# Performance work log

Measured on AMD Instinct MI355X. Metric: run time of the kernel, lower is better.

## Reference

```python
import jax, jax.numpy as jnp
import numpy as np

T, B, I, H, L, O = 512, 64, 128, 512, 2, 256


def _lstm_layer(x, Wih, Whh, b):
    """One LSTM layer over time. x:[T,B,in] -> (ys:[T,B,H], hT:[B,H], cT:[B,H]).
    PyTorch gate order: i, f, g, o. Zero initial state (module's zero buffers)."""
    Hs = Whh.shape[1]
    # Precompute input contribution for all timesteps (one big GEMM).
    xg = jnp.einsum('tbi,gi->tbg', x, Wih) + b  # [T,B,4H]

    def step(carry, xt):
        h, c = carry
        g = xt + h @ Whh.T  # [B,4H]
        i, f, gg, o = jnp.split(g, 4, axis=-1)
        c = jax.nn.sigmoid(f) * c + jax.nn.sigmoid(i) * jnp.tanh(gg)
        h = jax.nn.sigmoid(o) * jnp.tanh(c)
        return (h, c), h

    h0 = jnp.zeros((x.shape[1], Hs), x.dtype)
    (hT, cT), ys = jax.lax.scan(step, (h0, h0), xg)
    return ys, hT, cT


def setup_inputs() -> dict:
    key = jax.random.key(0)
    ks = jax.random.split(key, 9)
    s = 1.0 / np.sqrt(H)  # torch default uniform(-1/sqrt(H), 1/sqrt(H)) scale
    u = lambda k, shp: jax.random.uniform(k, shp, jnp.float32, -s, s)
    return {
        'x': jax.random.normal(ks[0], (T, B, I), jnp.float32),
        'W_ih0': u(ks[1], (4 * H, I)),
        'W_hh0': u(ks[2], (4 * H, H)),
        'b0': u(ks[3], (4 * H,)),  # b_ih + b_hh combined
        'W_ih1': u(ks[4], (4 * H, H)),
        'W_hh1': u(ks[5], (4 * H, H)),
        'b1': u(ks[6], (4 * H,)),
        'fc_w': u(ks[7], (O, H)),
        'fc_b': u(ks[8], (O,)),
    }


def reference(x, W_ih0, W_hh0, b0, W_ih1, W_hh1, b1, fc_w, fc_b):
    y0, h0, c0 = _lstm_layer(x, W_ih0, W_hh0, b0)
    y1, h1, c1 = _lstm_layer(y0, W_ih1, W_hh1, b1)
    fc = jnp.einsum('tbh,oh->tbo', y1, fc_w) + fc_b  # fused output projection
    hN = jnp.stack([h0, h1])  # [L,B,H]
    cN = jnp.stack([c0, c1])
    return fc, (hN, cN)
```

## Files before the change

kernel.cpp:

```cpp
#include <hip/hip_runtime.h>
#include <hip/hip_bf16.h>

#define T_SEQ 512
#define BATCH 64
#define IN0   128
#define HID   512
#define OUTF  256
#define G4    (4*HID)
#define NWG_L 64
#define FLAG_STRIDE 32

typedef __attribute__((ext_vector_type(8))) short short8;
typedef __attribute__((ext_vector_type(4))) float f32x4;
typedef unsigned short u16;

__device__ __forceinline__ float sigmoidf_(float x) { return 1.f / (1.f + __expf(-x)); }
__device__ __forceinline__ float tanhf_(float x)    { return 1.f - 2.f / (1.f + __expf(2.f * x)); }

__device__ __forceinline__ u16 f2bf(float f) {
    union { float f; unsigned u; } a; a.f = f;
    unsigned u = a.u;
    return (u16)((u + 0x7fffu + ((u >> 16) & 1u)) >> 16);
}

__device__ __forceinline__ void wave_poll_ge(unsigned* flags, int lane, unsigned tgt) {
    unsigned it = 0;
    for (;;) {
        unsigned v = __hip_atomic_load(flags + (size_t)lane * FLAG_STRIDE,
                                       __ATOMIC_RELAXED, __HIP_MEMORY_SCOPE_AGENT);
        if (__all((int)(v >= tgt))) return;
        __builtin_amdgcn_s_sleep(2);
        if ((++it & 2047u) == 0u)
            (void)__hip_atomic_load(flags, __ATOMIC_ACQUIRE, __HIP_MEMORY_SCOPE_AGENT);
    }
}

__global__ void cvt_f32_bf16(const float* __restrict__ in, u16* __restrict__ out, int n4) {
    int i = blockIdx.x * blockDim.x + threadIdx.x;
    if (i < n4) {
        float4 v = reinterpret_cast<const float4*>(in)[i];
        ushort4 o;
        o.x = f2bf(v.x); o.y = f2bf(v.y); o.z = f2bf(v.z); o.w = f2bf(v.w);
        reinterpret_cast<ushort4*>(out)[i] = o;
    }
}

template<int LAYER>
__device__ __forceinline__ void run_layer(
    const u16* __restrict__ asrc,
    const u16* __restrict__ wih, const u16* __restrict__ whh,
    const float* __restrict__ bias,
    u16* __restrict__ ybuf,
    float* __restrict__ hNout, float* __restrict__ cNout,
    unsigned* flags_own, unsigned* flags_dep, int g,
    u16 (*lds_w)[32][512], float (*lds_g)[33], float (*lds_b)[16])
{
    constexpr int KIN = (LAYER == 0) ? IN0 : HID;
    constexpr int KS1 = KIN / 32;
    constexpr int KS  = KS1 + 16;

    const int tid  = threadIdx.x;
    const int lane = tid & 63;
    const int w    = tid >> 6;
    const int ubase = 8 * g;

    for (int idx = tid; idx < 2 * KS * 64; idx += 256) {
        int nt  = (idx >= KS * 64) ? 1 : 0;
        int rem = idx - nt * KS * 64;
        int ks = rem >> 6, s = rem & 63, q = s & 15, kq = s >> 4;
        int r = (q >> 2) * HID + ubase + 4 * nt + (q & 3);
        const u16* src = (ks < KS1)
            ? wih + (size_t)r * KIN + (size_t)ks * 32 + kq * 8
            : whh + (size_t)r * HID + (size_t)(ks - KS1) * 32 + kq * 8;
        *reinterpret_cast<uint4*>(&lds_w[nt][ks][s * 8]) =
            *reinterpret_cast<const uint4*>(src);
    }
    if (tid < 32) {
        int nt = tid >> 4, q = tid & 15;
        lds_b[nt][q] = bias[(q >> 2) * HID + ubase + 4 * nt + (q & 3)];
    }
    __syncthreads();

    const int pb  = tid & 63;
    const int pu2 = tid >> 6;
    float c0 = 0.f, c1 = 0.f;

    const int arow = 16 * w + (lane & 15);
    const int koff = (lane >> 4) * 8;

    for (int t = 0; t < T_SEQ; ++t) {
        f32x4 ac0[4] = {{0,0,0,0},{0,0,0,0},{0,0,0,0},{0,0,0,0}};
        f32x4 ac1[4] = {{0,0,0,0},{0,0,0,0},{0,0,0,0},{0,0,0,0}};

        if (LAYER == 0) {
            const u16* ap = asrc + ((size_t)t * BATCH + arow) * KIN + koff;
            short8 a[KS1];
            #pragma unroll
            for (int j = 0; j < KS1; ++j)
                a[j] = *reinterpret_cast<const short8*>(ap + j * 32);
            #pragma unroll
            for (int j = 0; j < KS1; ++j) {
                ac0[j & 3] = __builtin_amdgcn_mfma_f32_16x16x32_bf16(
                    a[j], *reinterpret_cast<const short8*>(&lds_w[0][j][lane * 8]), ac0[j & 3], 0, 0, 0);
                ac1[j & 3] = __builtin_amdgcn_mfma_f32_16x16x32_bf16(
                    a[j], *reinterpret_cast<const short8*>(&lds_w[1][j][lane * 8]), ac1[j & 3], 0, 0, 0);
            }
        }

        if (LAYER == 0) {
            if (t > 0) {
                if (w == 0) wave_poll_ge(flags_own, lane, (unsigned)t);
                __syncthreads();
            }
        } else {
            if (w == 0) wave_poll_ge(flags_own, lane, (unsigned)t);
            if (w == 1) wave_poll_ge(flags_dep, lane, (unsigned)(t + 1));
            __syncthreads();
        }

        if (t > 0) {
            const u16* hp = ybuf + ((size_t)(t - 1) * BATCH + arow) * HID + koff;
            short8 a[16];
            #pragma unroll
            for (int j = 0; j < 16; ++j)
                a[j] = *reinterpret_cast<const short8*>(hp + j * 32);
            #pragma unroll
            for (int j = 0; j < 16; ++j) {
                ac0[j & 3] = __builtin_amdgcn_mfma_f32_16x16x32_bf16(
                    a[j], *reinterpret_cast<const short8*>(&lds_w[0][KS1 + j][lane * 8]), ac0[j & 3], 0, 0, 0);
                ac1[j & 3] = __builtin_amdgcn_mfma_f32_16x16x32_bf16(
                    a[j], *reinterpret_cast<const short8*>(&lds_w[1][KS1 + j][lane * 8]), ac1[j & 3], 0, 0, 0);
            }
        }

        if (LAYER == 1) {
            const u16* ap = asrc + ((size_t)t * BATCH + arow) * HID + koff;
            short8 a[16];
            #pragma unroll
            for (int j = 0; j < 16; ++j)
                a[j] = *reinterpret_cast<const short8*>(ap + j * 32);
            #pragma unroll
            for (int j = 0; j < 16; ++j) {
                ac0[j & 3] = __builtin_amdgcn_mfma_f32_16x16x32_bf16(
                    a[j], *reinterpret_cast<const short8*>(&lds_w[0][j][lane * 8]), ac0[j & 3], 0, 0, 0);
                ac1[j & 3] = __builtin_amdgcn_mfma_f32_16x16x32_bf16(
                    a[j], *reinterpret_cast<const short8*>(&lds_w[1][j][lane * 8]), ac1[j & 3], 0, 0, 0);
            }
        }

        f32x4 s0 = (ac0[0] + ac0[1]) + (ac0[2] + ac0[3]);
        f32x4 s1 = (ac1[0] + ac1[1]) + (ac1[2] + ac1[3]);
        #pragma unroll
        for (int j = 0; j < 4; ++j) {
            int row = 16 * w + (lane >> 4) * 4 + j;
            lds_g[row][lane & 15]        = s0[j];
            lds_g[row][16 + (lane & 15)] = s1[j];
        }
        __syncthreads();

        {
            const int nt = pu2 >> 1;
            const int dq = (2 * pu2) & 3;
            const float* gr = &lds_g[pb][nt * 16];
            const float* br = lds_b[nt];
            float gi0 = sigmoidf_(gr[dq]      + br[dq]);
            float gf0 = sigmoidf_(gr[4 + dq]  + br[4 + dq]);
            float gg0 = tanhf_(   gr[8 + dq]  + br[8 + dq]);
            float go0 = sigmoidf_(gr[12 + dq] + br[12 + dq]);
            c0 = gf0 * c0 + gi0 * gg0;
            float h0v = go0 * tanhf_(c0);
            float gi1 = sigmoidf_(gr[dq + 1]      + br[dq + 1]);
            float gf1 = sigmoidf_(gr[4 + dq + 1]  + br[4 + dq + 1]);
            float gg1 = tanhf_(   gr[8 + dq + 1]  + br[8 + dq + 1]);
            float go1 = sigmoidf_(gr[12 + dq + 1] + br[12 + dq + 1]);
            c1 = gf1 * c1 + gi1 * gg1;
            float h1v = go1 * tanhf_(c1);

            unsigned pack = (unsigned)f2bf(h0v) | ((unsigned)f2bf(h1v) << 16);
            unsigned* yp32 = reinterpret_cast<unsigned*>(ybuf)
                           + ((size_t)t * BATCH + pb) * (HID / 2) + (ubase + 2 * pu2) / 2;
            __hip_atomic_store(yp32, pack, __ATOMIC_RELAXED, __HIP_MEMORY_SCOPE_AGENT);

            if (t == T_SEQ - 1) {
                hNout[pb * HID + ubase + 2 * pu2]     = h0v;
                hNout[pb * HID + ubase + 2 * pu2 + 1] = h1v;
                cNout[pb * HID + ubase + 2 * pu2]     = c0;
                cNout[pb * HID + ubase + 2 * pu2 + 1] = c1;
            }
        }

        asm volatile("s_waitcnt vmcnt(0)" ::: "memory");
        __syncthreads();
        if (tid == 0)
            __hip_atomic_store(flags_own + (size_t)g * FLAG_STRIDE, (unsigned)(t + 1),
                               __ATOMIC_RELAXED, __HIP_MEMORY_SCOPE_AGENT);
    }
}

__global__ __launch_bounds__(256, 1)
void lstm_fused(const u16* __restrict__ x_bf,
                const u16* __restrict__ wih0, const u16* __restrict__ whh0, const float* __restrict__ b0,
                const u16* __restrict__ wih1, const u16* __restrict__ whh1, const float* __restrict__ b1,
                u16* __restrict__ y0, u16* __restrict__ y1,
                float* __restrict__ hN, float* __restrict__ cN,
                unsigned* __restrict__ ctr)
{
    __shared__ __align__(16) u16 lds_w[2][32][512];
    __shared__ float lds_g[BATCH][33];
    __shared__ float lds_b[2][16];

    unsigned* flags0 = ctr;
    unsigned* flags1 = ctr + NWG_L * FLAG_STRIDE;

    const int wgid = blockIdx.x;
    if (wgid < NWG_L) {
        run_layer<0>(x_bf, wih0, whh0, b0, y0, hN, cN,
                     flags0, flags0, wgid, lds_w, lds_g, lds_b);
    } else {
        run_layer<1>(y0, wih1, whh1, b1, y1, hN + BATCH * HID, cN + BATCH * HID,
                     flags1, flags0, wgid - NWG_L, lds_w, lds_g, lds_b);
    }
}

__global__ __launch_bounds__(256)
void fc_kernel(const u16* __restrict__ y1, const u16* __restrict__ fcw,
               const float* __restrict__ fcb, float* __restrict__ out)
{
    const int tid  = threadIdx.x;
    const int lane = tid & 63;
    const int wgid = blockIdx.x * 4 + (tid >> 6);
    const int nq   = wgid & 3;
    const int mt0  = wgid >> 2;

    for (int j = 0; j < 8; ++j) {
        int mt = mt0 + j * 256;
        f32x4 acc[4] = {{0,0,0,0},{0,0,0,0},{0,0,0,0},{0,0,0,0}};
        const u16* arow = y1 + ((size_t)mt * 16 + (lane & 15)) * HID + (lane >> 4) * 8;
        #pragma unroll
        for (int ks = 0; ks < 16; ++ks) {
            short8 a = *reinterpret_cast<const short8*>(arow + ks * 32);
            #pragma unroll
            for (int nt = 0; nt < 4; ++nt) {
                const u16* brow = fcw + ((size_t)(nq * 64 + nt * 16 + (lane & 15))) * HID
                                      + ks * 32 + (lane >> 4) * 8;
                short8 b = *reinterpret_cast<const short8*>(brow);
                acc[nt] = __builtin_amdgcn_mfma_f32_16x16x32_bf16(a, b, acc[nt], 0, 0, 0);
            }
        }
        #pragma unroll
        for (int nt = 0; nt < 4; ++nt) {
            int col = nq * 64 + nt * 16 + (lane & 15);
            float bb = fcb[col];
            #pragma unroll
            for (int jj = 0; jj < 4; ++jj) {
                int row = mt * 16 + (lane >> 4) * 4 + jj;
                out[(size_t)row * OUTF + col] = acc[nt][jj] + bb;
            }
        }
    }
}

extern "C" void kernel_launch(void* const* d_in, const int* in_sizes, int n_in,
                              void* d_out, int out_size, void* d_ws, size_t ws_size,
                              hipStream_t stream)
{
    const float* x    = (const float*)d_in[0];
    const float* wih0 = (const float*)d_in[1];
    const float* whh0 = (const float*)d_in[2];
    const float* b0   = (const float*)d_in[3];
    const float* wih1 = (const float*)d_in[4];
    const float* whh1 = (const float*)d_in[5];
    const float* b1   = (const float*)d_in[6];
    const float* fcw  = (const float*)d_in[7];
    const float* fcb  = (const float*)d_in[8];
    float* out = (float*)d_out;

    const size_t flag_bytes = (size_t)2 * NWG_L * FLAG_STRIDE * 4;

    char* ws = (char*)d_ws;
    size_t off = 0;
    unsigned* ctr = (unsigned*)ws;                    off += flag_bytes;
    u16* x_bf    = (u16*)(ws + off);                  off += (size_t)T_SEQ * BATCH * IN0 * 2;
    u16* wih0_bf = (u16*)(ws + off);                  off += (size_t)G4 * IN0 * 2;
    u16* whh0_bf = (u16*)(ws + off);                  off += (size_t)G4 * HID * 2;
    u16* wih1_bf = (u16*)(ws + off);                  off += (size_t)G4 * HID * 2;
    u16* whh1_bf = (u16*)(ws + off);                  off += (size_t)G4 * HID * 2;
    u16* fcw_bf  = (u16*)(ws + off);                  off += (size_t)OUTF * HID * 2;
    u16* y0      = (u16*)(ws + off);                  off += (size_t)T_SEQ * BATCH * HID * 2;
    u16* y1      = (u16*)(ws + off);                  off += (size_t)T_SEQ * BATCH * HID * 2;

    hipMemsetAsync(ctr, 0, flag_bytes, stream);

    auto conv = [&](const float* in, u16* o, int n) {
        int n4 = n / 4;
        cvt_f32_bf16<<<(n4 + 255) / 256, 256, 0, stream>>>(in, o, n4);
    };
    conv(x,    x_bf,    T_SEQ * BATCH * IN0);
    conv(wih0, wih0_bf, G4 * IN0);
    conv(whh0, whh0_bf, G4 * HID);
    conv(wih1, wih1_bf, G4 * HID);
    conv(whh1, whh1_bf, G4 * HID);
    conv(fcw,  fcw_bf,  OUTF * HID);

    float* outFC = out;
    float* hN = out + (size_t)T_SEQ * BATCH * OUTF;
    float* cN = hN + 2 * BATCH * HID;

    lstm_fused<<<2 * NWG_L, 256, 0, stream>>>(x_bf, wih0_bf, whh0_bf, b0,
                                              wih1_bf, whh1_bf, b1,
                                              y0, y1, hN, cN, ctr);
    fc_kernel<<<256, 256, 0, stream>>>(y1, fcw_bf, fcb, outFC);
}
```

Before: 3.669 ms.

## Pin each LSTM layer's workgroups to one XCD and poll flags via local L2

```diff
diff --git a/kernel.cpp b/kernel.cpp
--- a/kernel.cpp
+++ b/kernel.cpp
@@ -8,7 +8,7 @@
 #define OUTF  256
 #define G4    (4*HID)
 #define NWG_L 64
-#define FLAG_STRIDE 32
+#define FSTR  32
 
 typedef __attribute__((ext_vector_type(8))) short short8;
 typedef __attribute__((ext_vector_type(4))) float f32x4;
@@ -23,15 +23,36 @@
     return (u16)((u + 0x7fffu + ((u >> 16) & 1u)) >> 16);
 }
 
-__device__ __forceinline__ void wave_poll_ge(unsigned* flags, int lane, unsigned tgt) {
-    unsigned it = 0;
+__device__ __forceinline__ unsigned ld_flag_sc0(const unsigned* p) {
+    unsigned v;
+    asm volatile("global_load_dword %0, %1, off sc0\n\ts_waitcnt vmcnt(0)"
+                 : "=v"(v) : "v"(p) : "memory");
+    return v;
+}
+
+__device__ __forceinline__ void poll_local(const unsigned* lf, const unsigned* mf,
+                                           int lane, unsigned tgt) {
+    unsigned best = 0, it = 0;
     for (;;) {
-        unsigned v = __hip_atomic_load(flags + (size_t)lane * FLAG_STRIDE,
+        unsigned v = ld_flag_sc0(lf + (size_t)lane * FSTR);
+        best = v > best ? v : best;
+        if (__all((int)(best >= tgt))) return;
+        if ((++it & 15u) == 0u) {
+            unsigned m = __hip_atomic_load(mf + (size_t)lane * FSTR,
+                                           __ATOMIC_RELAXED, __HIP_MEMORY_SCOPE_AGENT);
+            best = m > best ? m : best;
+            if (__all((int)(best >= tgt))) return;
+        }
+        __builtin_amdgcn_s_sleep(1);
+    }
+}
+
+__device__ __forceinline__ void poll_agent(const unsigned* flags, int lane, unsigned tgt) {
+    for (;;) {
+        unsigned v = __hip_atomic_load(flags + (size_t)lane * FSTR,
                                        __ATOMIC_RELAXED, __HIP_MEMORY_SCOPE_AGENT);
         if (__all((int)(v >= tgt))) return;
         __builtin_amdgcn_s_sleep(2);
-        if ((++it & 2047u) == 0u)
-            (void)__hip_atomic_load(flags, __ATOMIC_ACQUIRE, __HIP_MEMORY_SCOPE_AGENT);
     }
 }
 
@@ -52,7 +73,10 @@
     const float* __restrict__ bias,
     u16* __restrict__ ybuf,
     float* __restrict__ hNout, float* __restrict__ cNout,
-    unsigned* flags_own, unsigned* flags_dep, int g,
+    unsigned* fl_own,
+    unsigned* fm_own,
+    unsigned* f_cross,
+    int g,
     u16 (*lds_w)[32][512], float (*lds_g)[33], float (*lds_b)[16])
 {
     constexpr int KIN = (LAYER == 0) ? IN0 : HID;
@@ -109,12 +133,12 @@
 
         if (LAYER == 0) {
             if (t > 0) {
-                if (w == 0) wave_poll_ge(flags_own, lane, (unsigned)t);
+                if (w == 0) poll_local(fl_own, fm_own, lane, (unsigned)t);
                 __syncthreads();
             }
         } else {
-            if (w == 0) wave_poll_ge(flags_own, lane, (unsigned)t);
-            if (w == 1) wave_poll_ge(flags_dep, lane, (unsigned)(t + 1));
+            if (w == 0 && t > 0) poll_local(fl_own, fm_own, lane, (unsigned)t);
+            if (w == 1) poll_agent(f_cross, lane, (unsigned)(t + 1));
             __syncthreads();
         }
 
@@ -158,6 +182,8 @@
         }
         __syncthreads();
 
+        unsigned pack;
+        unsigned* yp32;
         {
             const int nt = pu2 >> 1;
             const int dq = (2 * pu2) & 3;
@@ -176,10 +202,10 @@
             c1 = gf1 * c1 + gi1 * gg1;
             float h1v = go1 * tanhf_(c1);
 
-            unsigned pack = (unsigned)f2bf(h0v) | ((unsigned)f2bf(h1v) << 16);
-            unsigned* yp32 = reinterpret_cast<unsigned*>(ybuf)
-                           + ((size_t)t * BATCH + pb) * (HID / 2) + (ubase + 2 * pu2) / 2;
-            __hip_atomic_store(yp32, pack, __ATOMIC_RELAXED, __HIP_MEMORY_SCOPE_AGENT);
+            pack = (unsigned)f2bf(h0v) | ((unsigned)f2bf(h1v) << 16);
+            yp32 = reinterpret_cast<unsigned*>(ybuf)
+                 + ((size_t)t * BATCH + pb) * (HID / 2) + (ubase + 2 * pu2) / 2;
+            *yp32 = pack;
 
             if (t == T_SEQ - 1) {
                 hNout[pb * HID + ubase + 2 * pu2]     = h0v;
@@ -191,8 +217,22 @@
 
         asm volatile("s_waitcnt vmcnt(0)" ::: "memory");
         __syncthreads();
+        if (tid == 0) {
+            *(volatile unsigned*)(fl_own + (size_t)g * FSTR) = (unsigned)(t + 1);
+            __hip_atomic_store(fm_own + (size_t)g * FSTR, (unsigned)(t + 1),
+                               __ATOMIC_RELAXED, __HIP_MEMORY_SCOPE_AGENT);
+            if (LAYER == 0)
+                __hip_atomic_store(f_cross + (size_t)g * FSTR, (unsigned)t,
+                                   __ATOMIC_RELAXED, __HIP_MEMORY_SCOPE_AGENT);
+        }
+        if (LAYER == 0)
+            __hip_atomic_store(yp32, pack, __ATOMIC_RELAXED, __HIP_MEMORY_SCOPE_AGENT);
+    }
+
+    if (LAYER == 0) {
+        asm volatile("s_waitcnt vmcnt(0)" ::: "memory");
         if (tid == 0)
-            __hip_atomic_store(flags_own + (size_t)g * FLAG_STRIDE, (unsigned)(t + 1),
+            __hip_atomic_store(f_cross + (size_t)g * FSTR, (unsigned)T_SEQ,
                                __ATOMIC_RELAXED, __HIP_MEMORY_SCOPE_AGENT);
     }
 }
@@ -203,22 +243,58 @@
                 const u16* __restrict__ wih1, const u16* __restrict__ whh1, const float* __restrict__ b1,
                 u16* __restrict__ y0, u16* __restrict__ y1,
                 float* __restrict__ hN, float* __restrict__ cN,
-                unsigned* __restrict__ ctr)
+                unsigned* __restrict__ ctl)
 {
     __shared__ __align__(16) u16 lds_w[2][32][512];
     __shared__ float lds_g[BATCH][33];
     __shared__ float lds_b[2][16];
-
-    unsigned* flags0 = ctr;
-    unsigned* flags1 = ctr + NWG_L * FLAG_STRIDE;
-
-    const int wgid = blockIdx.x;
-    if (wgid < NWG_L) {
+    __shared__ int s_layer, s_role;
+
+    if (threadIdx.x == 0) {
+        unsigned xcc;
+        asm volatile("s_getreg_b32 %0, hwreg(HW_REG_XCC_ID)" : "=s"(xcc));
+        xcc &= 7u;
+        unsigned* pioneer = ctl + 0;
+        unsigned* lxcd    = ctl + 8;
+        unsigned* ltick   = ctl + 16;
+        unsigned* rtick   = ctl + 24;
+        if (__hip_atomic_fetch_add(&pioneer[xcc], 1u,
+                                   __ATOMIC_RELAXED, __HIP_MEMORY_SCOPE_AGENT) == 0u) {
+            unsigned li = __hip_atomic_fetch_add(ltick, 1u,
+                                                 __ATOMIC_RELAXED, __HIP_MEMORY_SCOPE_AGENT);
+            __hip_atomic_store(&lxcd[xcc], (li < 2u) ? (li + 1u) : 3u,
+                               __ATOMIC_RELAXED, __HIP_MEMORY_SCOPE_AGENT);
+        }
+        unsigned lx;
+        do {
+            lx = __hip_atomic_load(&lxcd[xcc], __ATOMIC_RELAXED, __HIP_MEMORY_SCOPE_AGENT);
+            if (lx == 0u) __builtin_amdgcn_s_sleep(1);
+        } while (lx == 0u);
+        int layer = (lx <= 2u) ? (int)lx - 1 : -1;
+        int role = -1;
+        if (layer >= 0) {
+            unsigned r = __hip_atomic_fetch_add(&rtick[layer], 1u,
+                                                __ATOMIC_RELAXED, __HIP_MEMORY_SCOPE_AGENT);
+            if (r < NWG_L) role = (int)r;
+        }
+        s_layer = layer; s_role = role;
+    }
+    __syncthreads();
+    const int layer = s_layer, role = s_role;
+    if (role < 0) return;
+
+    unsigned* flags0  = ctl + 64;
+    unsigned* flags1  = flags0  + NWG_L * FSTR;
+    unsigned* flags0m = flags1  + NWG_L * FSTR;
+    unsigned* flags1m = flags0m + NWG_L * FSTR;
+    unsigned* flags0r = flags1m + NWG_L * FSTR;
+
+    if (layer == 0) {
         run_layer<0>(x_bf, wih0, whh0, b0, y0, hN, cN,
-                     flags0, flags0, wgid, lds_w, lds_g, lds_b);
+                     flags0, flags0m, flags0r, role, lds_w, lds_g, lds_b);
     } else {
         run_layer<1>(y0, wih1, whh1, b1, y1, hN + BATCH * HID, cN + BATCH * HID,
-                     flags1, flags0, wgid - NWG_L, lds_w, lds_g, lds_b);
+                     flags1, flags1m, flags0r, role, lds_w, lds_g, lds_b);
     }
 }
 
@@ -275,11 +351,12 @@
     const float* fcb  = (const float*)d_in[8];
     float* out = (float*)d_out;
 
-    const size_t flag_bytes = (size_t)2 * NWG_L * FLAG_STRIDE * 4;
+    const size_t ctl_u32 = 64 + (size_t)5 * NWG_L * FSTR;
+    const size_t ctl_bytes = ctl_u32 * 4;
 
     char* ws = (char*)d_ws;
     size_t off = 0;
-    unsigned* ctr = (unsigned*)ws;                    off += flag_bytes;
+    unsigned* ctl = (unsigned*)ws;                    off += (ctl_bytes + 255) & ~(size_t)255;
     u16* x_bf    = (u16*)(ws + off);                  off += (size_t)T_SEQ * BATCH * IN0 * 2;
     u16* wih0_bf = (u16*)(ws + off);                  off += (size_t)G4 * IN0 * 2;
     u16* whh0_bf = (u16*)(ws + off);                  off += (size_t)G4 * HID * 2;
@@ -289,7 +366,7 @@
     u16* y0      = (u16*)(ws + off);                  off += (size_t)T_SEQ * BATCH * HID * 2;
     u16* y1      = (u16*)(ws + off);                  off += (size_t)T_SEQ * BATCH * HID * 2;
 
-    hipMemsetAsync(ctr, 0, flag_bytes, stream);
+    hipMemsetAsync(ctl, 0, ctl_bytes, stream);
 
     auto conv = [&](const float* in, u16* o, int n) {
         int n4 = n / 4;
@@ -306,8 +383,8 @@
     float* hN = out + (size_t)T_SEQ * BATCH * OUTF;
     float* cN = hN + 2 * BATCH * HID;
 
-    lstm_fused<<<2 * NWG_L, 256, 0, stream>>>(x_bf, wih0_bf, whh0_bf, b0,
-                                              wih1_bf, whh1_bf, b1,
-                                              y0, y1, hN, cN, ctr);
+    lstm_fused<<<1024, 256, 0, stream>>>(x_bf, wih0_bf, whh0_bf, b0,
+                                         wih1_bf, whh1_bf, b1,
+                                         y0, y1, hN, cN, ctl);
     fc_kernel<<<256, 256, 0, stream>>>(y1, fcw_bf, fcb, outFC);
 }
```

Measured after the change: 6.359 ms. 73.3% more time.
